# Kernel tuning notes

Hardware: AMD Instinct MI355X
Metric: run time of the kernel (lower is better)

Reference implementation:

```python
import jax, jax.numpy as jnp
import numpy as np

N_NODES = 100000
N_EDGES = 640000
F_IN = 128
HID = 128
N_CLASSES = 10
N_GRAPHS = 64


def _sage_conv(x, src, tgt, Wl, bl, Wr, num_nodes):
    # PyG SAGEConv (mean aggr): out = lin_l(mean_{j in N(i)} x_j) + lin_r(x_i)
    msg_sum = jax.ops.segment_sum(x[src], tgt, num_segments=num_nodes)      # [N, F]
    deg = jax.ops.segment_sum(jnp.ones((src.shape[0],), x.dtype), tgt,
                              num_segments=num_nodes)                        # [N]
    agg = msg_sum / jnp.maximum(deg, 1.0)[:, None]
    return agg @ Wl + bl + x @ Wr


def setup_inputs() -> dict:
    key = jax.random.key(0)
    ks = jax.random.split(key, 12)
    def lin(k, fan_in, fan_out):
        s = 1.0 / np.sqrt(fan_in)
        return jax.random.uniform(k, (fan_in, fan_out), jnp.float32, -s, s)
    x = jax.random.normal(ks[0], (N_NODES, F_IN), jnp.float32)
    edge_index = jax.random.randint(ks[1], (2, N_EDGES), 0, N_NODES, jnp.int64)
    batch = jnp.sort(jax.random.randint(ks[2], (N_NODES,), 0, N_GRAPHS, jnp.int64))
    return {
        "x": x, "edge_index": edge_index, "batch": batch,
        "W1l": lin(ks[3], F_IN, HID), "b1": jnp.zeros((HID,), jnp.float32), "W1r": lin(ks[4], F_IN, HID),
        "W2l": lin(ks[5], HID, HID), "b2": jnp.zeros((HID,), jnp.float32), "W2r": lin(ks[6], HID, HID),
        "W3l": lin(ks[7], HID, HID), "b3": jnp.zeros((HID,), jnp.float32), "W3r": lin(ks[8], HID, HID),
        "Wout": lin(ks[9], HID, N_CLASSES), "bout": jnp.zeros((N_CLASSES,), jnp.float32),
    }


def reference(x, edge_index, batch, W1l, b1, W1r, W2l, b2, W2r, W3l, b3, W3r, Wout, bout):
    src, tgt = edge_index[0], edge_index[1]
    n = x.shape[0]
    h = jax.nn.relu(_sage_conv(x, src, tgt, W1l, b1, W1r, n))
    h = jax.nn.relu(_sage_conv(h, src, tgt, W2l, b2, W2r, n))
    h = _sage_conv(h, src, tgt, W3l, b3, W3r, n)
    # global mean pool over graphs
    g_sum = jax.ops.segment_sum(h, batch, num_segments=N_GRAPHS)            # [G, H]
    g_cnt = jax.ops.segment_sum(jnp.ones((n,), h.dtype), batch, num_segments=N_GRAPHS)
    g = g_sum / jnp.maximum(g_cnt, 1.0)[:, None]
    # dropout is identity in eval mode
    return g @ Wout + bout
```

## Files before the change

kernel.cpp:

```cpp
#include <hip/hip_runtime.h>
#include <hip/hip_bf16.h>

#define N_NODES_C 100000
#define N_GRAPHS_C 64
#define FDIM 128
#define NPB 512
#define NBUCK 196
#define SB 256
#define CAP 4096

typedef _Float16 half8v __attribute__((ext_vector_type(8)));
typedef __attribute__((ext_vector_type(4))) float f32x4;

__device__ __forceinline__ unsigned short f2h(float f) {
    union { _Float16 h; unsigned short u; } v; v.h = (_Float16)f; return v.u;
}

__device__ __forceinline__ void acc8h(float* a, half8v v) {
#pragma unroll
    for (int j = 0; j < 8; ++j) a[j] += (float)v[j];
}

__global__ __launch_bounds__(256) void fused_scatter(const int* __restrict__ src,
                                                     const int* __restrict__ tgt,
                                                     int* __restrict__ cur,
                                                     uint2* __restrict__ staged, int E) {
    __shared__ int lcnt[NBUCK];
    __shared__ int lbase[NBUCK];
    const int t = threadIdx.x;
    const int blk = blockIdx.x;
    if (t < NBUCK) lcnt[t] = 0;
    __syncthreads();
    const int chunk = (E + SB - 1) / SB;
    const int base = blk * chunk;
    const int lim = min(E, base + chunk);
    for (int e = base + t; e < lim; e += 256)
        atomicAdd(&lcnt[tgt[e] >> 9], 1);
    __syncthreads();
    if (t < NBUCK) {
        int c = lcnt[t];
        lbase[t] = c ? atomicAdd(&cur[t], c) : 0;
        lcnt[t] = 0;
    }
    __syncthreads();
    for (int e = base + t; e < lim; e += 256) {
        int tv = tgt[e];
        int b = tv >> 9;
        int r = atomicAdd(&lcnt[b], 1);
        int pos = lbase[b] + r;
        if (pos < CAP) {
            uint2 p; p.x = (unsigned)tv; p.y = (unsigned)src[e];
            staged[(size_t)b * CAP + pos] = p;
        }
    }
}

__global__ __launch_bounds__(256) void bucket_finalize(const uint2* __restrict__ staged,
                                                       const int* __restrict__ cur,
                                                       int2* __restrict__ rsbe,
                                                       float* __restrict__ invd,
                                                       int* __restrict__ csr, int N) {
    __shared__ int dcnt[NPB];
    __shared__ int pref[NPB];
    __shared__ int ts[256];
    const int t = threadIdx.x;
    const int b = blockIdx.x;
    const int s = b * CAP;
    const int e = s + min(cur[b], CAP);
    const int nb0 = b * NPB;
    const int nn = min(NPB, N - nb0);

    dcnt[t] = 0; dcnt[t + 256] = 0;
    __syncthreads();
    for (int i = s + t; i < e; i += 256)
        atomicAdd(&dcnt[(int)staged[i].x - nb0], 1);
    __syncthreads();

    int a0 = dcnt[2 * t], a1 = dcnt[2 * t + 1];
    ts[t] = a0 + a1;
    __syncthreads();
    for (int off = 1; off < 256; off <<= 1) {
        int u = (t >= off) ? ts[t - off] : 0;
        __syncthreads();
        ts[t] += u;
        __syncthreads();
    }
    int excl = (t > 0) ? ts[t - 1] : 0;
    pref[2 * t] = excl;
    pref[2 * t + 1] = excl + a0;
    __syncthreads();

    if (t < nn) {
        int bg = s + pref[t];
        rsbe[nb0 + t] = make_int2(bg, bg + dcnt[t]);
        invd[nb0 + t] = 1.0f / (float)max(dcnt[t], 1);
    }
    int t2 = t + 256;
    if (t2 < nn) {
        int bg = s + pref[t2];
        rsbe[nb0 + t2] = make_int2(bg, bg + dcnt[t2]);
        invd[nb0 + t2] = 1.0f / (float)max(dcnt[t2], 1);
    }
    __syncthreads();

    dcnt[t] = pref[t]; dcnt[t + 256] = pref[t + 256];
    __syncthreads();
    for (int i = s + t; i < e; i += 256) {
        uint2 p = staged[i];
        int r = atomicAdd(&dcnt[(int)p.x - nb0], 1);
        csr[s + r] = (int)p.y;
    }
}

__device__ __forceinline__ void prep_w_body(const float* __restrict__ Wl,
                                            const float* __restrict__ Wr,
                                            unsigned short* __restrict__ outW, int id) {
    int c = id >> 9, i = id & 511;
    int l = i >> 3, e = i & 7;
    int khalf = c >> 5, nf = (c >> 2) & 7, ks4 = c & 3;
    int j = nf * 16 + (l & 15);
    int k = khalf * 128 + ks4 * 32 + ((l >> 4) << 3) + e;
    float w = (k < 128) ? Wl[k * 128 + j] : Wr[(k - 128) * 128 + j];
    outW[id] = f2h(w);
}

__global__ __launch_bounds__(256) void prep_all(const float* __restrict__ x,
                                                unsigned short* __restrict__ B0, int n8,
                                                const float* __restrict__ W1l,
                                                const float* __restrict__ W1r,
                                                unsigned short* __restrict__ wt1,
                                                const float* __restrict__ W2l,
                                                const float* __restrict__ W2r,
                                                unsigned short* __restrict__ wt2,
                                                const int* __restrict__ batch,
                                                int* __restrict__ gstart,
                                                float* __restrict__ gcnt,
                                                float* __restrict__ pa,
                                                float* __restrict__ ph,
                                                int* __restrict__ cur,
                                                int nNodes, int convBlocks) {
    const int b = blockIdx.x;
    const int t = threadIdx.x;
    if (b < convBlocks) {
        int i = b * 256 + t;
        if (i < n8) {
            float4 v0 = *(const float4*)(x + (size_t)i * 8);
            float4 v1 = *(const float4*)(x + (size_t)i * 8 + 4);
            half8v o;
            o[0] = (_Float16)v0.x; o[1] = (_Float16)v0.y; o[2] = (_Float16)v0.z; o[3] = (_Float16)v0.w;
            o[4] = (_Float16)v1.x; o[5] = (_Float16)v1.y; o[6] = (_Float16)v1.z; o[7] = (_Float16)v1.w;
            *(half8v*)(B0 + (size_t)i * 8) = o;
        }
    } else if (b < convBlocks + 128) {
        prep_w_body(W1l, W1r, wt1, (b - convBlocks) * 256 + t);
    } else if (b < convBlocks + 256) {
        prep_w_body(W2l, W2r, wt2, (b - convBlocks - 128) * 256 + t);
    } else {
        if (t < 64) {
            int g = t;
            int lo = 0, hi = nNodes;
            while (lo < hi) { int m = (lo + hi) >> 1; if (batch[m] < g) lo = m + 1; else hi = m; }
            int lb = lo;
            lo = 0; hi = nNodes;
            while (lo < hi) { int m = (lo + hi) >> 1; if (batch[m] < g + 1) lo = m + 1; else hi = m; }
            gstart[g] = lb;
            gcnt[g] = (float)(lo - lb);
            if (g == 0) gstart[64] = nNodes;
        }
        for (int i = t; i < N_GRAPHS_C * FDIM; i += 256) { pa[i] = 0.f; ph[i] = 0.f; }
        for (int i = t; i < NBUCK; i += 256) cur[i] = 0;
    }
}

__global__ __launch_bounds__(512) void sage_layer(const unsigned short* __restrict__ Xin,
                                                  const unsigned short* __restrict__ WtF,
                                                  const float* __restrict__ bias,
                                                  const int* __restrict__ csr,
                                                  const int2* __restrict__ rsbe,
                                                  const float* __restrict__ invd,
                                                  unsigned short* __restrict__ Hout, int N) {
    __shared__ unsigned short atile[128 * 128];
    __shared__ unsigned short wlds[32 * 512];

    const int t = threadIdx.x;
    const int r0 = blockIdx.x * 128;

#pragma unroll
    for (int rep = 0; rep < 4; ++rep) {
        int e = rep * 4096 + t * 8;
        *(half8v*)&wlds[e] = *(const half8v*)(WtF + e);
    }

    {
        const int grp = t >> 4, lane = t & 15;
        const half8v vzero = (half8v)(_Float16)0;
#pragma unroll
        for (int it = 0; it < 4; ++it) {
            const int row = it * 32 + grp;
            const int node = r0 + row;
            float a[8] = {0.f, 0.f, 0.f, 0.f, 0.f, 0.f, 0.f, 0.f};
            if (node < N) {
                const int2 be = rsbe[node];
                const int beg = be.x, end = be.y;
                for (int base = beg; base < end; base += 8) {
                    const int cnt = end - base;
                    int idx[8];
#pragma unroll
                    for (int k = 0; k < 8; ++k) idx[k] = csr[min(base + k, end - 1)];
                    half8v v[8];
#pragma unroll
                    for (int k = 0; k < 8; ++k)
                        v[k] = *(const half8v*)(Xin + ((size_t)idx[k] << 7) + lane * 8);
#pragma unroll
                    for (int k = 0; k < 8; ++k) {
                        half8v vv = (k < cnt) ? v[k] : vzero;
                        acc8h(a, vv);
                    }
                }
                float sc = invd[node];
#pragma unroll
                for (int j = 0; j < 8; ++j) a[j] *= sc;
            }
            half8v o;
#pragma unroll
            for (int j = 0; j < 8; ++j) o[j] = (_Float16)a[j];
            const int chunk = lane ^ (row & 7);
            *(half8v*)&atile[row * 128 + chunk * 8] = o;
        }
    }
    __syncthreads();

    const int wave = t >> 6, l = t & 63;
    const int trow = wave * 16 + (l & 15);
    const int lk = (l >> 4) << 3;

    f32x4 acc[8];
#pragma unroll
    for (int nf = 0; nf < 8; ++nf) acc[nf] = (f32x4)(0.f);

#pragma unroll
    for (int ks4 = 0; ks4 < 4; ++ks4) {
        const int chunk = (ks4 * 4 + (l >> 4)) ^ (trow & 7);
        half8v af = *(const half8v*)&atile[trow * 128 + chunk * 8];
#pragma unroll
        for (int nf = 0; nf < 8; ++nf) {
            half8v bh = *(const half8v*)&wlds[(nf * 4 + ks4) * 512 + l * 8];
            acc[nf] = __builtin_amdgcn_mfma_f32_16x16x32_f16(bh, af, acc[nf], 0, 0, 0);
        }
    }
    __syncthreads();
#pragma unroll
    for (int rep = 0; rep < 4; ++rep) {
        int e = rep * 4096 + t * 8;
        *(half8v*)&wlds[e] = *(const half8v*)(WtF + 16384 + e);
    }
    __syncthreads();

    {
        int row = r0 + trow;
        if (row >= N) row = N - 1;
#pragma unroll
        for (int ks4 = 0; ks4 < 4; ++ks4) {
            half8v af = *(const half8v*)(Xin + ((size_t)row << 7) + ks4 * 32 + lk);
#pragma unroll
            for (int nf = 0; nf < 8; ++nf) {
                half8v bh = *(const half8v*)&wlds[(nf * 4 + ks4) * 512 + l * 8];
                acc[nf] = __builtin_amdgcn_mfma_f32_16x16x32_f16(bh, af, acc[nf], 0, 0, 0);
            }
        }
    }

    const int jb = (l >> 4) << 2;
    const int orow = r0 + trow;
    if (orow < N) {
#pragma unroll
        for (int nf = 0; nf < 8; ++nf) {
            float4 bv = *(const float4*)&bias[nf * 16 + jb];
            unsigned short h0 = f2h(fmaxf(acc[nf][0] + bv.x, 0.f));
            unsigned short h1 = f2h(fmaxf(acc[nf][1] + bv.y, 0.f));
            unsigned short h2 = f2h(fmaxf(acc[nf][2] + bv.z, 0.f));
            unsigned short h3 = f2h(fmaxf(acc[nf][3] + bv.w, 0.f));
            uint2 st;
            st.x = (unsigned)h0 | ((unsigned)h1 << 16);
            st.y = (unsigned)h2 | ((unsigned)h3 << 16);
            *(uint2*)(Hout + ((size_t)orow << 7) + nf * 16 + jb) = st;
        }
    }
}

__global__ __launch_bounds__(256) void agg3_pool(const unsigned short* __restrict__ H2,
                                                 const int* __restrict__ csr,
                                                 const int2* __restrict__ rsbe,
                                                 const float* __restrict__ invd,
                                                 const int* __restrict__ gstart,
                                                 float* __restrict__ pa,
                                                 float* __restrict__ ph) {
    const int g = blockIdx.x >> 4;
    const int q = blockIdx.x & 15;
    const int s = gstart[g], e = gstart[g + 1];
    const int len = e - s;
    const int cs = s + (len * q) / 16;
    const int ce = s + (len * (q + 1)) / 16;
    const int t = threadIdx.x;
    const int grp = t >> 4, lane = t & 15;

    float aacc[8] = {0.f, 0.f, 0.f, 0.f, 0.f, 0.f, 0.f, 0.f};
    float hacc[8] = {0.f, 0.f, 0.f, 0.f, 0.f, 0.f, 0.f, 0.f};
    const half8v vzero = (half8v)(_Float16)0;

    for (int node = cs + grp; node < ce; node += 16) {
        const int2 be = rsbe[node];
        const int beg = be.x, end = be.y;
        float a[8] = {0.f, 0.f, 0.f, 0.f, 0.f, 0.f, 0.f, 0.f};
        for (int base = beg; base < end; base += 8) {
            const int cnt = end - base;
            int idx[8];
#pragma unroll
            for (int k = 0; k < 8; ++k) idx[k] = csr[min(base + k, end - 1)];
            half8v v[8];
#pragma unroll
            for (int k = 0; k < 8; ++k)
                v[k] = *(const half8v*)(H2 + ((size_t)idx[k] << 7) + lane * 8);
#pragma unroll
            for (int k = 0; k < 8; ++k) {
                half8v vv = (k < cnt) ? v[k] : vzero;
                acc8h(a, vv);
            }
        }
        const float sc = invd[node];
#pragma unroll
        for (int j = 0; j < 8; ++j) aacc[j] += a[j] * sc;
        half8v own = *(const half8v*)(H2 + ((size_t)node << 7) + lane * 8);
        acc8h(hacc, own);
    }

    __shared__ float red[16][128];
#pragma unroll
    for (int j = 0; j < 8; ++j) red[grp][lane * 8 + j] = aacc[j];
    __syncthreads();
    if (t < 128) {
        float sum = 0.f;
#pragma unroll
        for (int k = 0; k < 16; ++k) sum += red[k][t];
        unsafeAtomicAdd(&pa[g * 128 + t], sum);
    }
    __syncthreads();
#pragma unroll
    for (int j = 0; j < 8; ++j) red[grp][lane * 8 + j] = hacc[j];
    __syncthreads();
    if (t < 128) {
        float sum = 0.f;
#pragma unroll
        for (int k = 0; k < 16; ++k) sum += red[k][t];
        unsafeAtomicAdd(&ph[g * 128 + t], sum);
    }
}

__global__ __launch_bounds__(128) void final_fused(const float* __restrict__ pa,
                                                   const float* __restrict__ ph,
                                                   const float* __restrict__ gcnt,
                                                   const float* __restrict__ W3l,
                                                   const float* __restrict__ W3r,
                                                   const float* __restrict__ b3,
                                                   const float* __restrict__ Wout,
                                                   const float* __restrict__ bout,
                                                   float* __restrict__ out) {
    __shared__ float sA[FDIM], sH[FDIM], sT[FDIM];
    int g = blockIdx.x;
    int j = threadIdx.x;
    float inv = 1.0f / fmaxf(gcnt[g], 1.0f);
    sA[j] = pa[g * FDIM + j] * inv;
    sH[j] = ph[g * FDIM + j] * inv;
    __syncthreads();
    float acc = b3[j];
    for (int c = 0; c < FDIM; ++c)
        acc += sA[c] * W3l[c * FDIM + j] + sH[c] * W3r[c * FDIM + j];
    sT[j] = acc;
    __syncthreads();
    if (j < 10) {
        float o = bout[j];
        for (int c = 0; c < FDIM; ++c) o += sT[c] * Wout[c * 10 + j];
        out[g * 10 + j] = o;
    }
}

extern "C" void kernel_launch(void* const* d_in, const int* in_sizes, int n_in,
                              void* d_out, int out_size, void* d_ws, size_t ws_size,
                              hipStream_t stream) {
    const float* x     = (const float*)d_in[0];
    const int*   edge  = (const int*)d_in[1];
    const int*   batch = (const int*)d_in[2];
    const float* W1l = (const float*)d_in[3];
    const float* b1  = (const float*)d_in[4];
    const float* W1r = (const float*)d_in[5];
    const float* W2l = (const float*)d_in[6];
    const float* b2  = (const float*)d_in[7];
    const float* W2r = (const float*)d_in[8];
    const float* W3l = (const float*)d_in[9];
    const float* b3  = (const float*)d_in[10];
    const float* W3r = (const float*)d_in[11];
    const float* Wout = (const float*)d_in[12];
    const float* bout = (const float*)d_in[13];
    float* out = (float*)d_out;

    const int N = N_NODES_C;
    const int E = in_sizes[1] / 2;
    const int* src = edge;
    const int* tgt = edge + E;

    char* ws = (char*)d_ws;
    size_t off = 0;
    auto carve = [&](size_t bytes) { char* p = ws + off; off += (bytes + 255) & ~(size_t)255; return p; };
    int2*  rsbe = (int2*)carve((size_t)N * 8);
    float* invd = (float*)carve((size_t)N * 4);
    int*   gstart = (int*)carve(65 * 4);
    float* gcnt = (float*)carve(64 * 4);
    float* pa   = (float*)carve((size_t)N_GRAPHS_C * FDIM * 4);
    float* ph   = (float*)carve((size_t)N_GRAPHS_C * FDIM * 4);
    int*   cur  = (int*)carve(NBUCK * 4);
    unsigned short* wt1 = (unsigned short*)carve(32768 * 2);
    unsigned short* wt2 = (unsigned short*)carve(32768 * 2);
    uint2* staged = (uint2*)carve((size_t)NBUCK * CAP * 8);
    int*   csr  = (int*)carve((size_t)NBUCK * CAP * 4);
    unsigned short* B0 = (unsigned short*)carve((size_t)N * FDIM * 2);
    unsigned short* B2 = (unsigned short*)carve((size_t)N * FDIM * 2);

    const int n8 = N * FDIM / 8;
    const int convBlocks = (n8 + 255) / 256;
    prep_all<<<convBlocks + 257, 256, 0, stream>>>(x, B0, n8,
                                                   W1l, W1r, wt1, W2l, W2r, wt2,
                                                   batch, gstart, gcnt, pa, ph, cur,
                                                   N, convBlocks);

    fused_scatter<<<SB, 256, 0, stream>>>(src, tgt, cur, staged, E);
    bucket_finalize<<<NBUCK, 256, 0, stream>>>(staged, cur, rsbe, invd, csr, N);

    const int layerGrid = (N + 127) / 128;

    sage_layer<<<layerGrid, 512, 0, stream>>>(B0, wt1, b1, csr, rsbe, invd, B2, N);
    sage_layer<<<layerGrid, 512, 0, stream>>>(B2, wt2, b2, csr, rsbe, invd, B0, N);

    agg3_pool<<<N_GRAPHS_C * 16, 256, 0, stream>>>(B0, csr, rsbe, invd, gstart, pa, ph);

    final_fused<<<N_GRAPHS_C, 128, 0, stream>>>(pa, ph, gcnt, W3l, W3r, b3, Wout, bout, out);
}
```

Measured before the change: 200.7 us.

## Gather neighbor features from FP8 copies and merge prep with edge scatter

Each layer now writes an extra FP8 copy of its node features, and the neighbor-mean gathers read 8 bytes per lane instead of 16. This is meant to halve the random-gather traffic that dominates aggregation. The prep kernel and the edge-bucketing scatter are merged into one launch, and the bucket counter reset moves to a memset. The cost is reduced precision in the aggregated messages and extra FP8 stores per layer.

```diff
diff --git a/kernel.cpp b/kernel.cpp
--- a/kernel.cpp
+++ b/kernel.cpp
@@ -11,6 +11,7 @@
 
 typedef _Float16 half8v __attribute__((ext_vector_type(8)));
 typedef __attribute__((ext_vector_type(4))) float f32x4;
+typedef __attribute__((ext_vector_type(2))) float f32x2;
 
 __device__ __forceinline__ unsigned short f2h(float f) {
     union { _Float16 h; unsigned short u; } v; v.h = (_Float16)f; return v.u;
@@ -21,37 +22,113 @@
     for (int j = 0; j < 8; ++j) a[j] += (float)v[j];
 }
 
-__global__ __launch_bounds__(256) void fused_scatter(const int* __restrict__ src,
-                                                     const int* __restrict__ tgt,
-                                                     int* __restrict__ cur,
-                                                     uint2* __restrict__ staged, int E) {
+__device__ __forceinline__ unsigned pk4fp8(float a, float b, float c, float d) {
+    int w = 0;
+    w = __builtin_amdgcn_cvt_pk_fp8_f32(a, b, w, false);
+    w = __builtin_amdgcn_cvt_pk_fp8_f32(c, d, w, true);
+    return (unsigned)w;
+}
+__device__ __forceinline__ void acc8fp8(float* a, uint2 v) {
+    f32x2 f0 = __builtin_amdgcn_cvt_pk_f32_fp8(v.x, false);
+    f32x2 f1 = __builtin_amdgcn_cvt_pk_f32_fp8(v.x, true);
+    f32x2 f2 = __builtin_amdgcn_cvt_pk_f32_fp8(v.y, false);
+    f32x2 f3 = __builtin_amdgcn_cvt_pk_f32_fp8(v.y, true);
+    a[0] += f0.x; a[1] += f0.y; a[2] += f1.x; a[3] += f1.y;
+    a[4] += f2.x; a[5] += f2.y; a[6] += f3.x; a[7] += f3.y;
+}
+
+__device__ __forceinline__ void prep_w_body(const float* __restrict__ Wl,
+                                            const float* __restrict__ Wr,
+                                            unsigned short* __restrict__ outW, int id) {
+    int c = id >> 9, i = id & 511;
+    int l = i >> 3, e = i & 7;
+    int khalf = c >> 5, nf = (c >> 2) & 7, ks4 = c & 3;
+    int j = nf * 16 + (l & 15);
+    int k = khalf * 128 + ks4 * 32 + ((l >> 4) << 3) + e;
+    float w = (k < 128) ? Wl[k * 128 + j] : Wr[(k - 128) * 128 + j];
+    outW[id] = f2h(w);
+}
+
+__global__ __launch_bounds__(256) void prep_scatter(const int* __restrict__ src,
+                                                    const int* __restrict__ tgt,
+                                                    int* __restrict__ cur,
+                                                    uint2* __restrict__ staged, int E,
+                                                    const float* __restrict__ x,
+                                                    unsigned short* __restrict__ B0,
+                                                    unsigned char* __restrict__ B08, int n8,
+                                                    const float* __restrict__ W1l,
+                                                    const float* __restrict__ W1r,
+                                                    unsigned short* __restrict__ wt1,
+                                                    const float* __restrict__ W2l,
+                                                    const float* __restrict__ W2r,
+                                                    unsigned short* __restrict__ wt2,
+                                                    const int* __restrict__ batch,
+                                                    int* __restrict__ gstart,
+                                                    float* __restrict__ gcnt,
+                                                    float* __restrict__ pa,
+                                                    float* __restrict__ ph,
+                                                    int nNodes, int convBlocks) {
     __shared__ int lcnt[NBUCK];
     __shared__ int lbase[NBUCK];
+    const int b = blockIdx.x;
     const int t = threadIdx.x;
-    const int blk = blockIdx.x;
-    if (t < NBUCK) lcnt[t] = 0;
-    __syncthreads();
-    const int chunk = (E + SB - 1) / SB;
-    const int base = blk * chunk;
-    const int lim = min(E, base + chunk);
-    for (int e = base + t; e < lim; e += 256)
-        atomicAdd(&lcnt[tgt[e] >> 9], 1);
-    __syncthreads();
-    if (t < NBUCK) {
-        int c = lcnt[t];
-        lbase[t] = c ? atomicAdd(&cur[t], c) : 0;
-        lcnt[t] = 0;
-    }
-    __syncthreads();
-    for (int e = base + t; e < lim; e += 256) {
-        int tv = tgt[e];
-        int b = tv >> 9;
-        int r = atomicAdd(&lcnt[b], 1);
-        int pos = lbase[b] + r;
-        if (pos < CAP) {
-            uint2 p; p.x = (unsigned)tv; p.y = (unsigned)src[e];
-            staged[(size_t)b * CAP + pos] = p;
-        }
+
+    if (b < SB) {
+        if (t < NBUCK) lcnt[t] = 0;
+        __syncthreads();
+        const int chunk = (E + SB - 1) / SB;
+        const int base = b * chunk;
+        const int lim = min(E, base + chunk);
+        for (int e = base + t; e < lim; e += 256)
+            atomicAdd(&lcnt[tgt[e] >> 9], 1);
+        __syncthreads();
+        if (t < NBUCK) {
+            int c = lcnt[t];
+            lbase[t] = c ? atomicAdd(&cur[t], c) : 0;
+            lcnt[t] = 0;
+        }
+        __syncthreads();
+        for (int e = base + t; e < lim; e += 256) {
+            int tv = tgt[e];
+            int bk = tv >> 9;
+            int r = atomicAdd(&lcnt[bk], 1);
+            int pos = lbase[bk] + r;
+            if (pos < CAP) {
+                uint2 p; p.x = (unsigned)tv; p.y = (unsigned)src[e];
+                staged[(size_t)bk * CAP + pos] = p;
+            }
+        }
+    } else if (b < SB + 128) {
+        prep_w_body(W1l, W1r, wt1, (b - SB) * 256 + t);
+    } else if (b < SB + 256) {
+        prep_w_body(W2l, W2r, wt2, (b - SB - 128) * 256 + t);
+    } else if (b < SB + 256 + convBlocks) {
+        int i = (b - SB - 256) * 256 + t;
+        if (i < n8) {
+            float4 v0 = *(const float4*)(x + (size_t)i * 8);
+            float4 v1 = *(const float4*)(x + (size_t)i * 8 + 4);
+            half8v o;
+            o[0] = (_Float16)v0.x; o[1] = (_Float16)v0.y; o[2] = (_Float16)v0.z; o[3] = (_Float16)v0.w;
+            o[4] = (_Float16)v1.x; o[5] = (_Float16)v1.y; o[6] = (_Float16)v1.z; o[7] = (_Float16)v1.w;
+            *(half8v*)(B0 + (size_t)i * 8) = o;
+            uint2 p8;
+            p8.x = pk4fp8(v0.x, v0.y, v0.z, v0.w);
+            p8.y = pk4fp8(v1.x, v1.y, v1.z, v1.w);
+            *(uint2*)(B08 + (size_t)i * 8) = p8;
+        }
+    } else {
+        if (t < 64) {
+            int g = t;
+            int lo = 0, hi = nNodes;
+            while (lo < hi) { int m = (lo + hi) >> 1; if (batch[m] < g) lo = m + 1; else hi = m; }
+            int lb = lo;
+            lo = 0; hi = nNodes;
+            while (lo < hi) { int m = (lo + hi) >> 1; if (batch[m] < g + 1) lo = m + 1; else hi = m; }
+            gstart[g] = lb;
+            gcnt[g] = (float)(lo - lb);
+            if (g == 0) gstart[64] = nNodes;
+        }
+        for (int i = t; i < N_GRAPHS_C * FDIM; i += 256) { pa[i] = 0.f; ph[i] = 0.f; }
     }
 }
 
@@ -112,73 +189,15 @@
     }
 }
 
-__device__ __forceinline__ void prep_w_body(const float* __restrict__ Wl,
-                                            const float* __restrict__ Wr,
-                                            unsigned short* __restrict__ outW, int id) {
-    int c = id >> 9, i = id & 511;
-    int l = i >> 3, e = i & 7;
-    int khalf = c >> 5, nf = (c >> 2) & 7, ks4 = c & 3;
-    int j = nf * 16 + (l & 15);
-    int k = khalf * 128 + ks4 * 32 + ((l >> 4) << 3) + e;
-    float w = (k < 128) ? Wl[k * 128 + j] : Wr[(k - 128) * 128 + j];
-    outW[id] = f2h(w);
-}
-
-__global__ __launch_bounds__(256) void prep_all(const float* __restrict__ x,
-                                                unsigned short* __restrict__ B0, int n8,
-                                                const float* __restrict__ W1l,
-                                                const float* __restrict__ W1r,
-                                                unsigned short* __restrict__ wt1,
-                                                const float* __restrict__ W2l,
-                                                const float* __restrict__ W2r,
-                                                unsigned short* __restrict__ wt2,
-                                                const int* __restrict__ batch,
-                                                int* __restrict__ gstart,
-                                                float* __restrict__ gcnt,
-                                                float* __restrict__ pa,
-                                                float* __restrict__ ph,
-                                                int* __restrict__ cur,
-                                                int nNodes, int convBlocks) {
-    const int b = blockIdx.x;
-    const int t = threadIdx.x;
-    if (b < convBlocks) {
-        int i = b * 256 + t;
-        if (i < n8) {
-            float4 v0 = *(const float4*)(x + (size_t)i * 8);
-            float4 v1 = *(const float4*)(x + (size_t)i * 8 + 4);
-            half8v o;
-            o[0] = (_Float16)v0.x; o[1] = (_Float16)v0.y; o[2] = (_Float16)v0.z; o[3] = (_Float16)v0.w;
-            o[4] = (_Float16)v1.x; o[5] = (_Float16)v1.y; o[6] = (_Float16)v1.z; o[7] = (_Float16)v1.w;
-            *(half8v*)(B0 + (size_t)i * 8) = o;
-        }
-    } else if (b < convBlocks + 128) {
-        prep_w_body(W1l, W1r, wt1, (b - convBlocks) * 256 + t);
-    } else if (b < convBlocks + 256) {
-        prep_w_body(W2l, W2r, wt2, (b - convBlocks - 128) * 256 + t);
-    } else {
-        if (t < 64) {
-            int g = t;
-            int lo = 0, hi = nNodes;
-            while (lo < hi) { int m = (lo + hi) >> 1; if (batch[m] < g) lo = m + 1; else hi = m; }
-            int lb = lo;
-            lo = 0; hi = nNodes;
-            while (lo < hi) { int m = (lo + hi) >> 1; if (batch[m] < g + 1) lo = m + 1; else hi = m; }
-            gstart[g] = lb;
-            gcnt[g] = (float)(lo - lb);
-            if (g == 0) gstart[64] = nNodes;
-        }
-        for (int i = t; i < N_GRAPHS_C * FDIM; i += 256) { pa[i] = 0.f; ph[i] = 0.f; }
-        for (int i = t; i < NBUCK; i += 256) cur[i] = 0;
-    }
-}
-
 __global__ __launch_bounds__(512) void sage_layer(const unsigned short* __restrict__ Xin,
+                                                  const unsigned char* __restrict__ X8in,
                                                   const unsigned short* __restrict__ WtF,
                                                   const float* __restrict__ bias,
                                                   const int* __restrict__ csr,
                                                   const int2* __restrict__ rsbe,
                                                   const float* __restrict__ invd,
-                                                  unsigned short* __restrict__ Hout, int N) {
+                                                  unsigned short* __restrict__ Hout,
+                                                  unsigned char* __restrict__ H8out, int N) {
     __shared__ unsigned short atile[128 * 128];
     __shared__ unsigned short wlds[32 * 512];
 
@@ -193,7 +212,6 @@
 
     {
         const int grp = t >> 4, lane = t & 15;
-        const half8v vzero = (half8v)(_Float16)0;
 #pragma unroll
         for (int it = 0; it < 4; ++it) {
             const int row = it * 32 + grp;
@@ -207,15 +225,16 @@
                     int idx[8];
 #pragma unroll
                     for (int k = 0; k < 8; ++k) idx[k] = csr[min(base + k, end - 1)];
-                    half8v v[8];
+                    uint2 v[8];
 #pragma unroll
                     for (int k = 0; k < 8; ++k)
-                        v[k] = *(const half8v*)(Xin + ((size_t)idx[k] << 7) + lane * 8);
+                        v[k] = *(const uint2*)(X8in + ((size_t)idx[k] << 7) + lane * 8);
+                    float tmp[8];
 #pragma unroll
                     for (int k = 0; k < 8; ++k) {
-                        half8v vv = (k < cnt) ? v[k] : vzero;
-                        acc8h(a, vv);
+                        if (k < cnt) acc8fp8(a, v[k]);
                     }
+                    (void)tmp;
                 }
                 float sc = invd[node];
 #pragma unroll
@@ -276,19 +295,21 @@
 #pragma unroll
         for (int nf = 0; nf < 8; ++nf) {
             float4 bv = *(const float4*)&bias[nf * 16 + jb];
-            unsigned short h0 = f2h(fmaxf(acc[nf][0] + bv.x, 0.f));
-            unsigned short h1 = f2h(fmaxf(acc[nf][1] + bv.y, 0.f));
-            unsigned short h2 = f2h(fmaxf(acc[nf][2] + bv.z, 0.f));
-            unsigned short h3 = f2h(fmaxf(acc[nf][3] + bv.w, 0.f));
+            float o0 = fmaxf(acc[nf][0] + bv.x, 0.f);
+            float o1 = fmaxf(acc[nf][1] + bv.y, 0.f);
+            float o2 = fmaxf(acc[nf][2] + bv.z, 0.f);
+            float o3 = fmaxf(acc[nf][3] + bv.w, 0.f);
             uint2 st;
-            st.x = (unsigned)h0 | ((unsigned)h1 << 16);
-            st.y = (unsigned)h2 | ((unsigned)h3 << 16);
+            st.x = (unsigned)f2h(o0) | ((unsigned)f2h(o1) << 16);
+            st.y = (unsigned)f2h(o2) | ((unsigned)f2h(o3) << 16);
             *(uint2*)(Hout + ((size_t)orow << 7) + nf * 16 + jb) = st;
+            *(unsigned*)(H8out + ((size_t)orow << 7) + nf * 16 + jb) = pk4fp8(o0, o1, o2, o3);
         }
     }
 }
 
 __global__ __launch_bounds__(256) void agg3_pool(const unsigned short* __restrict__ H2,
+                                                 const unsigned char* __restrict__ H28,
                                                  const int* __restrict__ csr,
                                                  const int2* __restrict__ rsbe,
                                                  const float* __restrict__ invd,
@@ -306,7 +327,6 @@
 
     float aacc[8] = {0.f, 0.f, 0.f, 0.f, 0.f, 0.f, 0.f, 0.f};
     float hacc[8] = {0.f, 0.f, 0.f, 0.f, 0.f, 0.f, 0.f, 0.f};
-    const half8v vzero = (half8v)(_Float16)0;
 
     for (int node = cs + grp; node < ce; node += 16) {
         const int2 be = rsbe[node];
@@ -317,14 +337,13 @@
             int idx[8];
 #pragma unroll
             for (int k = 0; k < 8; ++k) idx[k] = csr[min(base + k, end - 1)];
-            half8v v[8];
+            uint2 v[8];
 #pragma unroll
             for (int k = 0; k < 8; ++k)
-                v[k] = *(const half8v*)(H2 + ((size_t)idx[k] << 7) + lane * 8);
+                v[k] = *(const uint2*)(H28 + ((size_t)idx[k] << 7) + lane * 8);
 #pragma unroll
             for (int k = 0; k < 8; ++k) {
-                half8v vv = (k < cnt) ? v[k] : vzero;
-                acc8h(a, vv);
+                if (k < cnt) acc8fp8(a, v[k]);
             }
         }
         const float sc = invd[node];
@@ -424,23 +443,26 @@
     int*   csr  = (int*)carve((size_t)NBUCK * CAP * 4);
     unsigned short* B0 = (unsigned short*)carve((size_t)N * FDIM * 2);
     unsigned short* B2 = (unsigned short*)carve((size_t)N * FDIM * 2);
-
+    unsigned char* F0 = (unsigned char*)carve((size_t)N * FDIM);
+    unsigned char* F1 = (unsigned char*)carve((size_t)N * FDIM);
+
+    hipMemsetAsync(cur, 0, NBUCK * 4, stream);
     const int n8 = N * FDIM / 8;
     const int convBlocks = (n8 + 255) / 256;
-    prep_all<<<convBlocks + 257, 256, 0, stream>>>(x, B0, n8,
-                                                   W1l, W1r, wt1, W2l, W2r, wt2,
-                                                   batch, gstart, gcnt, pa, ph, cur,
-                                                   N, convBlocks);
-
-    fused_scatter<<<SB, 256, 0, stream>>>(src, tgt, cur, staged, E);
+    prep_scatter<<<SB + 256 + convBlocks + 1, 256, 0, stream>>>(
+        src, tgt, cur, staged, E,
+        x, B0, F0, n8,
+        W1l, W1r, wt1, W2l, W2r, wt2,
+        batch, gstart, gcnt, pa, ph, N, convBlocks);
+
     bucket_finalize<<<NBUCK, 256, 0, stream>>>(staged, cur, rsbe, invd, csr, N);
 
     const int layerGrid = (N + 127) / 128;
 
-    sage_layer<<<layerGrid, 512, 0, stream>>>(B0, wt1, b1, csr, rsbe, invd, B2, N);
-    sage_layer<<<layerGrid, 512, 0, stream>>>(B2, wt2, b2, csr, rsbe, invd, B0, N);
-
-    agg3_pool<<<N_GRAPHS_C * 16, 256, 0, stream>>>(B0, csr, rsbe, invd, gstart, pa, ph);
+    sage_layer<<<layerGrid, 512, 0, stream>>>(B0, F0, wt1, b1, csr, rsbe, invd, B2, F1, N);
+    sage_layer<<<layerGrid, 512, 0, stream>>>(B2, F1, wt2, b2, csr, rsbe, invd, B0, F0, N);
+
+    agg3_pool<<<N_GRAPHS_C * 16, 256, 0, stream>>>(B0, F0, csr, rsbe, invd, gstart, pa, ph);
 
     final_fused<<<N_GRAPHS_C, 128, 0, stream>>>(pa, ph, gcnt, W3l, W3r, b3, Wout, bout, out);
 }
```

Result: faster. 193.8 us (-3.4%).
